# Kernel tuning notes

Hardware: AMD Instinct MI355X
Metric: run time of the kernel (lower is better)

The kernel has to match this reference:

```python
import jax, jax.numpy as jnp
import numpy as np

B, T, I, H, L = 64, 1024, 256, 512, 2

def setup_inputs() -> dict:
    key = jax.random.key(0)
    ks = jax.random.split(key, 1 + 4 * L)
    inp = {"x": jax.random.normal(ks[0], (B, 1, I, T), dtype=jnp.float32)}
    s_in = 1.0 / np.sqrt(H)
    for l in range(L):
        in_dim = I if l == 0 else H
        k0, k1, k2, k3 = ks[1 + 4 * l: 5 + 4 * l]
        inp[f"W_ih{l}"] = jax.random.uniform(k0, (4 * H, in_dim), jnp.float32, -s_in, s_in)
        inp[f"W_hh{l}"] = jax.random.uniform(k1, (4 * H, H), jnp.float32, -s_in, s_in)
        inp[f"b_ih{l}"] = jax.random.uniform(k2, (4 * H,), jnp.float32, -s_in, s_in)
        inp[f"b_hh{l}"] = jax.random.uniform(k3, (4 * H,), jnp.float32, -s_in, s_in)
    return inp

def _lstm_layer(x, W_ih, W_hh, b_ih, b_hh):
    # x: [B, T, in_dim] -> outputs [B, T, H], (h_T, c_T) each [B, H]
    xp = jnp.einsum('bti,gi->btg', x, W_ih) + b_ih + b_hh  # [B, T, 4H]
    h0 = jnp.zeros((x.shape[0], H), x.dtype)
    c0 = jnp.zeros((x.shape[0], H), x.dtype)

    def step(carry, xt):
        h, c = carry
        gates = xt + h @ W_hh.T  # [B, 4H]
        i, f, g, o = jnp.split(gates, 4, axis=-1)  # PyTorch gate order: i,f,g,o
        i = jax.nn.sigmoid(i); f = jax.nn.sigmoid(f)
        g = jnp.tanh(g); o = jax.nn.sigmoid(o)
        c = f * c + i * g
        h = o * jnp.tanh(c)
        return (h, c), h

    (hT, cT), ys = jax.lax.scan(step, (h0, c0), jnp.swapaxes(xp, 0, 1))
    return jnp.swapaxes(ys, 0, 1), hT, cT

def reference(x, W_ih0, W_hh0, b_ih0, b_hh0, W_ih1, W_hh1, b_ih1, b_hh1):
    # x: [B, 1, I, T] -> squeeze(1), permute(0,2,1) -> [B, T, I]
    seq = jnp.transpose(jnp.squeeze(x, 1), (0, 2, 1))
    params = [(W_ih0, W_hh0, b_ih0, b_hh0), (W_ih1, W_hh1, b_ih1, b_hh1)]
    hs, cs = [], []
    out = seq
    for (W_ih, W_hh, b_ih, b_hh) in params:
        out, hT, cT = _lstm_layer(out, W_ih, W_hh, b_ih, b_hh)
        hs.append(hT); cs.append(cT)
    hidden = jnp.stack(hs, 0)  # [L, B, H]
    cell = jnp.stack(cs, 0)    # [L, B, H]
    return (out, (hidden, cell))
```

## Files before the change

kernel.cpp:

```cpp
#include <hip/hip_runtime.h>

#define HB 64
#define HT 1024
#define HI 256
#define HH 512

typedef short short8 __attribute__((ext_vector_type(8)));
typedef float f32x4 __attribute__((ext_vector_type(4)));

__device__ __forceinline__ unsigned short f2bf(float f) {
    unsigned u = __float_as_uint(f);
    u += 0x7FFF + ((u >> 16) & 1);
    return (unsigned short)(u >> 16);
}
__device__ __forceinline__ float bf2f(unsigned short s) {
    return __uint_as_float(((unsigned)s) << 16);
}
__device__ __forceinline__ float fsigmoid(float x) {
    return __builtin_amdgcn_rcpf(1.0f + __expf(-x));
}
__device__ __forceinline__ float ftanh(float x) {
    return 1.0f - 2.0f * __builtin_amdgcn_rcpf(__expf(2.0f * x) + 1.0f);
}

__device__ __forceinline__ short8 ld_frag(const unsigned long long* p) {
    union { unsigned long long u[2]; short8 s; } cv;
    cv.u[0] = __hip_atomic_load(p,     __ATOMIC_RELAXED, __HIP_MEMORY_SCOPE_AGENT);
    cv.u[1] = __hip_atomic_load(p + 1, __ATOMIC_RELAXED, __HIP_MEMORY_SCOPE_AGENT);
    return cv.s;
}

__global__ void pack_weights(const float* __restrict__ Wih0, const float* __restrict__ Whh0,
                             const float* __restrict__ bih0, const float* __restrict__ bhh0,
                             const float* __restrict__ Wih1, const float* __restrict__ Whh1,
                             const float* __restrict__ bih1, const float* __restrict__ bhh1,
                             unsigned short* __restrict__ wp0,
                             unsigned short* __restrict__ wp1,
                             float* __restrict__ bs) {
    int idx = blockIdx.x * 256 + threadIdx.x;
    int stride = gridDim.x * 256;
    const int NP0 = 128 * 24 * 512;
    const int NP1 = 128 * 32 * 512;
    for (int e = idx; e < NP0; e += stride) {
        int j = e & 7, l = (e >> 3) & 63, rem = e >> 9;
        int kt = rem % 24, nt = rem / 24;
        int n = nt * 16 + (l & 15);
        int k = kt * 32 + ((l >> 4) << 3) + j;
        float v = (k < HI) ? Wih0[n * HI + k] : Whh0[n * HH + (k - HI)];
        wp0[e] = f2bf(v);
    }
    for (int e = idx; e < NP1; e += stride) {
        int j = e & 7, l = (e >> 3) & 63, rem = e >> 9;
        int kt = rem & 31, nt = rem >> 5;
        int n = nt * 16 + (l & 15);
        int k = kt * 32 + ((l >> 4) << 3) + j;
        float v = (k < HH) ? Wih1[n * HH + k] : Whh1[n * HH + (k - HH)];
        wp1[e] = f2bf(v);
    }
    for (int e = idx; e < 2048; e += stride) {
        bs[e]        = bih0[e] + bhh0[e];
        bs[2048 + e] = bih1[e] + bhh1[e];
    }
}

__global__ void pack_x(const float* __restrict__ x, unsigned short* __restrict__ xp) {
    int tt = blockIdx.x;
    int ii = blockIdx.y;
    int bt = blockIdx.z;
    int w  = threadIdx.x;
    __shared__ unsigned short tile[512][16];
    int tloc = w & 15;
    for (int q = 0; q < 32; ++q) {
        int p = q * 16 + (w >> 4);
        int m = p >> 5, iloc = p & 31;
        int b = bt * 16 + m, i = ii * 32 + iloc, t = tt * 16 + tloc;
        tile[p][tloc] = f2bf(x[((size_t)b * HI + i) * HT + t]);
    }
    __syncthreads();
    int e  = w * 2;
    int l  = e >> 3, j0 = e & 7;
    int m  = l & 15;
    int i0 = ((l >> 4) << 3) + j0;
    for (int ti = 0; ti < 16; ++ti) {
        int t = tt * 16 + ti;
        size_t base = ((size_t)(t * 4 + bt) * 8 + ii) * 512;
        unsigned v0 = tile[m * 32 + i0][ti];
        unsigned v1 = tile[m * 32 + i0 + 1][ti];
        ((unsigned int*)xp)[(base + e) >> 1] = v0 | (v1 << 16);
    }
}

__global__ void init_flags(int* __restrict__ f, int n) {
    int idx = blockIdx.x * 256 + threadIdx.x;
    for (int e = idx; e < n; e += gridDim.x * 256) f[e] = 0;
}

__global__ void __launch_bounds__(256, 1) lstm_persist(
        const unsigned short* __restrict__ wp0,
        const unsigned short* __restrict__ wp1,
        const float* __restrict__ bs,
        const unsigned short* __restrict__ xp,
        unsigned long long* __restrict__ h0ring,
        unsigned long long* __restrict__ h1ring,
        int* __restrict__ flag0,
        int* __restrict__ flag1,
        float* __restrict__ out) {
    __shared__ int4 ldsw[8192];
    __shared__ unsigned long long stage[256];

    const int bid   = blockIdx.x;
    const int layer = bid >> 5;
    const int ut    = bid & 31;
    const int tid   = threadIdx.x;
    const int mt    = tid >> 6;
    const int l     = tid & 63;
    const int ul    = l & 15;
    const int q     = l >> 4;
    const int KT    = layer ? 32 : 24;

    const short8* ldsf = (const short8*)ldsw;
    unsigned short* stage_s = (unsigned short*)stage;

    {
        const unsigned short* wsrc = layer ? wp1 : wp0;
        for (int g = 0; g < 4; ++g) {
            const int4* src = (const int4*)(wsrc + (size_t)(g * 32 + ut) * KT * 512);
            int4* dst = ldsw + (size_t)g * KT * 64;
            for (int i = tid; i < KT * 64; i += 256) dst[i] = src[i];
        }
    }
    float bv[4];
    #pragma unroll
    for (int g = 0; g < 4; ++g) bv[g] = bs[layer * 2048 + g * HH + ut * 16 + ul];
    float cc[4] = {0.f, 0.f, 0.f, 0.f};
    __syncthreads();

    const int u = ut * 16 + ul;
    const int stg_w = mt * 256 + (ul >> 3) * 128 + (ul & 7);
    const size_t ring_dst_sub = (size_t)(tid >> 6) * 2048 +
                                (ut >> 1) * 128 + ((2 * ut) & 3) * 32 + (tid & 63);

    for (int t = 0; t < HT; ++t) {
        f32x4 acc[4];
        #pragma unroll
        for (int g = 0; g < 4; ++g) {
            f32x4 a; a[0] = bv[g]; a[1] = bv[g]; a[2] = bv[g]; a[3] = bv[g];
            acc[g] = a;
        }

        if (layer == 0) {
            const short8* xa = (const short8*)xp + ((size_t)t * 4 + mt) * 8 * 64;
            #pragma unroll
            for (int kt = 0; kt < 8; ++kt) {
                short8 a = xa[kt * 64 + l];
                #pragma unroll
                for (int g = 0; g < 4; ++g)
                    acc[g] = __builtin_amdgcn_mfma_f32_16x16x32_bf16(
                        a, ldsf[(g * 24 + kt) * 64 + l], acc[g], 0, 0, 0);
            }
            if (t > 0) {
                if (tid < 64) {
                    const int* p;
                    bool skip;
                    if (l < 32) { p = flag0 + (size_t)(t - 1) * 32 + l; skip = false; }
                    else        { p = flag1 + (size_t)(t >= 8 ? t - 8 : 0) * 32 + (l - 32);
                                  skip = (t < 8); }
                    for (;;) {
                        int v = skip ? 1 : __hip_atomic_load(p, __ATOMIC_RELAXED,
                                                             __HIP_MEMORY_SCOPE_AGENT);
                        if (__ballot(v != 0) == ~0ull) break;
                        __builtin_amdgcn_s_sleep(1);
                    }
                }
                __syncthreads();
                const unsigned long long* hb =
                    h0ring + ((size_t)(((t - 1) & 7) * 4 + mt)) * 2048;
                short8 af[16];
                #pragma unroll
                for (int kt = 0; kt < 16; ++kt) af[kt] = ld_frag(hb + kt * 128 + l * 2);
                #pragma unroll
                for (int kt = 0; kt < 16; ++kt) {
                    #pragma unroll
                    for (int g = 0; g < 4; ++g)
                        acc[g] = __builtin_amdgcn_mfma_f32_16x16x32_bf16(
                            af[kt], ldsf[(g * 24 + 8 + kt) * 64 + l], acc[g], 0, 0, 0);
                }
            }
        } else {
            if (t > 0) {
                if (tid < 64) {
                    const int* p = flag1 + (size_t)(t - 1) * 32 + (l & 31);
                    while (__ballot(__hip_atomic_load(p, __ATOMIC_RELAXED,
                                    __HIP_MEMORY_SCOPE_AGENT) != 0) != ~0ull)
                        __builtin_amdgcn_s_sleep(1);
                }
                __syncthreads();
                const unsigned long long* hb =
                    h1ring + ((size_t)(((t - 1) & 1) * 4 + mt)) * 2048;
                short8 af[16];
                #pragma unroll
                for (int kt = 0; kt < 16; ++kt) af[kt] = ld_frag(hb + kt * 128 + l * 2);
                #pragma unroll
                for (int kt = 0; kt < 16; ++kt) {
                    #pragma unroll
                    for (int g = 0; g < 4; ++g)
                        acc[g] = __builtin_amdgcn_mfma_f32_16x16x32_bf16(
                            af[kt], ldsf[(g * 32 + 16 + kt) * 64 + l], acc[g], 0, 0, 0);
                }
            }
            if (tid < 64) {
                const int* p = flag0 + (size_t)t * 32 + (l & 31);
                while (__ballot(__hip_atomic_load(p, __ATOMIC_RELAXED,
                                __HIP_MEMORY_SCOPE_AGENT) != 0) != ~0ull)
                    __builtin_amdgcn_s_sleep(1);
            }
            __syncthreads();
            const unsigned long long* hb =
                h0ring + ((size_t)((t & 7) * 4 + mt)) * 2048;
            short8 af[16];
            #pragma unroll
            for (int kt = 0; kt < 16; ++kt) af[kt] = ld_frag(hb + kt * 128 + l * 2);
            #pragma unroll
            for (int kt = 0; kt < 16; ++kt) {
                #pragma unroll
                for (int g = 0; g < 4; ++g)
                    acc[g] = __builtin_amdgcn_mfma_f32_16x16x32_bf16(
                        af[kt], ldsf[(g * 32 + kt) * 64 + l], acc[g], 0, 0, 0);
            }
        }

        #pragma unroll
        for (int r = 0; r < 4; ++r) {
            int m = q * 4 + r;
            int b = mt * 16 + m;
            float iv = fsigmoid(acc[0][r]);
            float fv = fsigmoid(acc[1][r]);
            float gv = ftanh(acc[2][r]);
            float ov = fsigmoid(acc[3][r]);
            float c = fv * cc[r] + iv * gv;
            cc[r] = c;
            float h = ov * ftanh(c);
            stage_s[stg_w + m * 8] = f2bf(h);
            if (t == HT - 1) {
                out[33554432 + layer * 32768 + b * 512 + u] = h;
                out[33619968 + layer * 32768 + b * 512 + u] = c;
            }
        }
        __syncthreads();

        {
            unsigned long long v = stage[tid];
            unsigned long long* ring = layer ? h1ring : h0ring;
            int slot = layer ? (t & 1) : (t & 7);
            __hip_atomic_store(ring + (size_t)slot * 8192 + ring_dst_sub, v,
                               __ATOMIC_RELAXED, __HIP_MEMORY_SCOPE_AGENT);
        }
        if (layer == 1) {
            int b = tid >> 2, ch = tid & 3;
            const unsigned short* sp = stage_s + (b >> 4) * 256 + (ch >> 1) * 128 +
                                       (b & 15) * 8 + (ch & 1) * 4;
            f32x4 o;
            o[0] = bf2f(sp[0]); o[1] = bf2f(sp[1]);
            o[2] = bf2f(sp[2]); o[3] = bf2f(sp[3]);
            *(f32x4*)&out[((size_t)b * HT + t) * HH + ut * 16 + ch * 4] = o;
        }

        asm volatile("s_waitcnt vmcnt(0)" ::: "memory");
        __syncthreads();
        if (tid == 0) {
            int* fl = layer ? flag1 : flag0;
            __hip_atomic_store(fl + (size_t)t * 32 + ut, 1,
                               __ATOMIC_RELAXED, __HIP_MEMORY_SCOPE_AGENT);
        }
    }
}

extern "C" void kernel_launch(void* const* d_in, const int* in_sizes, int n_in,
                              void* d_out, int out_size, void* d_ws, size_t ws_size,
                              hipStream_t stream) {
    const float* x    = (const float*)d_in[0];
    const float* Wih0 = (const float*)d_in[1];
    const float* Whh0 = (const float*)d_in[2];
    const float* bih0 = (const float*)d_in[3];
    const float* bhh0 = (const float*)d_in[4];
    const float* Wih1 = (const float*)d_in[5];
    const float* Whh1 = (const float*)d_in[6];
    const float* bih1 = (const float*)d_in[7];
    const float* bhh1 = (const float*)d_in[8];

    char* ws = (char*)d_ws;
    unsigned short* wp0 = (unsigned short*)(ws + 0);
    unsigned short* wp1 = (unsigned short*)(ws + 3145728);
    float*          bsv = (float*)(ws + 7340032);
    unsigned short* xp  = (unsigned short*)(ws + 7356416);
    int*   flag0        = (int*)(ws + 40910848);
    int*   flag1        = (int*)(ws + 41041920);
    unsigned long long* h0r = (unsigned long long*)(ws + 41172992);
    unsigned long long* h1r = (unsigned long long*)(ws + 41697280);
    float* out = (float*)d_out;

    pack_weights<<<2048, 256, 0, stream>>>(Wih0, Whh0, bih0, bhh0,
                                           Wih1, Whh1, bih1, bhh1, wp0, wp1, bsv);
    pack_x<<<dim3(64, 8, 4), 256, 0, stream>>>(x, xp);
    init_flags<<<64, 256, 0, stream>>>(flag0, 65536);

    lstm_persist<<<64, 256, 0, stream>>>(wp0, wp1, bsv, xp, h0r, h1r,
                                         flag0, flag1, out);
}
```

Measured before the change: 7.203 ms.

## Merge layer-1 flag waits into one poll and publish flags before output store

New measurement: 8.787 ms. 22.0% more time.

```diff
diff --git a/kernel.cpp b/kernel.cpp
--- a/kernel.cpp
+++ b/kernel.cpp
@@ -187,45 +187,59 @@
                 }
             }
         } else {
+            if (tid < 64) {
+                const int* p;
+                bool skip;
+                if (l < 32) { p = flag0 + (size_t)t * 32 + l; skip = false; }
+                else        { p = flag1 + (size_t)(t > 0 ? t - 1 : 0) * 32 + (l - 32);
+                              skip = (t == 0); }
+                for (;;) {
+                    int v = skip ? 1 : __hip_atomic_load(p, __ATOMIC_RELAXED,
+                                                         __HIP_MEMORY_SCOPE_AGENT);
+                    if (__ballot(v != 0) == ~0ull) break;
+                    __builtin_amdgcn_s_sleep(1);
+                }
+            }
+            __syncthreads();
+
             if (t > 0) {
-                if (tid < 64) {
-                    const int* p = flag1 + (size_t)(t - 1) * 32 + (l & 31);
-                    while (__ballot(__hip_atomic_load(p, __ATOMIC_RELAXED,
-                                    __HIP_MEMORY_SCOPE_AGENT) != 0) != ~0ull)
-                        __builtin_amdgcn_s_sleep(1);
-                }
-                __syncthreads();
-                const unsigned long long* hb =
+                const unsigned long long* hb1 =
                     h1ring + ((size_t)(((t - 1) & 1) * 4 + mt)) * 2048;
-                short8 af[16];
-                #pragma unroll
-                for (int kt = 0; kt < 16; ++kt) af[kt] = ld_frag(hb + kt * 128 + l * 2);
+                const unsigned long long* hb0 =
+                    h0ring + ((size_t)((t & 7) * 4 + mt)) * 2048;
+                short8 af1[16];
+                short8 af0[16];
+                #pragma unroll
+                for (int kt = 0; kt < 16; ++kt) af1[kt] = ld_frag(hb1 + kt * 128 + l * 2);
+                #pragma unroll
+                for (int kt = 0; kt < 16; ++kt) af0[kt] = ld_frag(hb0 + kt * 128 + l * 2);
                 #pragma unroll
                 for (int kt = 0; kt < 16; ++kt) {
                     #pragma unroll
                     for (int g = 0; g < 4; ++g)
                         acc[g] = __builtin_amdgcn_mfma_f32_16x16x32_bf16(
-                            af[kt], ldsf[(g * 32 + 16 + kt) * 64 + l], acc[g], 0, 0, 0);
-                }
-            }
-            if (tid < 64) {
-                const int* p = flag0 + (size_t)t * 32 + (l & 31);
-                while (__ballot(__hip_atomic_load(p, __ATOMIC_RELAXED,
-                                __HIP_MEMORY_SCOPE_AGENT) != 0) != ~0ull)
-                    __builtin_amdgcn_s_sleep(1);
-            }
-            __syncthreads();
-            const unsigned long long* hb =
-                h0ring + ((size_t)((t & 7) * 4 + mt)) * 2048;
-            short8 af[16];
-            #pragma unroll
-            for (int kt = 0; kt < 16; ++kt) af[kt] = ld_frag(hb + kt * 128 + l * 2);
-            #pragma unroll
-            for (int kt = 0; kt < 16; ++kt) {
-                #pragma unroll
-                for (int g = 0; g < 4; ++g)
-                    acc[g] = __builtin_amdgcn_mfma_f32_16x16x32_bf16(
-                        af[kt], ldsf[(g * 32 + kt) * 64 + l], acc[g], 0, 0, 0);
+                            af1[kt], ldsf[(g * 32 + 16 + kt) * 64 + l], acc[g], 0, 0, 0);
+                }
+                #pragma unroll
+                for (int kt = 0; kt < 16; ++kt) {
+                    #pragma unroll
+                    for (int g = 0; g < 4; ++g)
+                        acc[g] = __builtin_amdgcn_mfma_f32_16x16x32_bf16(
+                            af0[kt], ldsf[(g * 32 + kt) * 64 + l], acc[g], 0, 0, 0);
+                }
+            } else {
+                const unsigned long long* hb0 =
+                    h0ring + ((size_t)((t & 7) * 4 + mt)) * 2048;
+                short8 af0[16];
+                #pragma unroll
+                for (int kt = 0; kt < 16; ++kt) af0[kt] = ld_frag(hb0 + kt * 128 + l * 2);
+                #pragma unroll
+                for (int kt = 0; kt < 16; ++kt) {
+                    #pragma unroll
+                    for (int g = 0; g < 4; ++g)
+                        acc[g] = __builtin_amdgcn_mfma_f32_16x16x32_bf16(
+                            af0[kt], ldsf[(g * 32 + kt) * 64 + l], acc[g], 0, 0, 0);
+                }
             }
         }
 
@@ -255,6 +269,15 @@
             __hip_atomic_store(ring + (size_t)slot * 8192 + ring_dst_sub, v,
                                __ATOMIC_RELAXED, __HIP_MEMORY_SCOPE_AGENT);
         }
+
+        asm volatile("s_waitcnt vmcnt(0)" ::: "memory");
+        __syncthreads();
+        if (tid == 0) {
+            int* fl = layer ? flag1 : flag0;
+            __hip_atomic_store(fl + (size_t)t * 32 + ut, 1,
+                               __ATOMIC_RELAXED, __HIP_MEMORY_SCOPE_AGENT);
+        }
+
         if (layer == 1) {
             int b = tid >> 2, ch = tid & 3;
             const unsigned short* sp = stage_s + (b >> 4) * 256 + (ch >> 1) * 128 +
@@ -263,14 +286,6 @@
             o[0] = bf2f(sp[0]); o[1] = bf2f(sp[1]);
             o[2] = bf2f(sp[2]); o[3] = bf2f(sp[3]);
             *(f32x4*)&out[((size_t)b * HT + t) * HH + ut * 16 + ch * 4] = o;
-        }
-
-        asm volatile("s_waitcnt vmcnt(0)" ::: "memory");
-        __syncthreads();
-        if (tid == 0) {
-            int* fl = layer ? flag1 : flag0;
-            __hip_atomic_store(fl + (size_t)t * 32 + ut, 1,
-                               __ATOMIC_RELAXED, __HIP_MEMORY_SCOPE_AGENT);
         }
     }
 }
```
